# Performance work log

Hardware: AMD Instinct MI355X
Metric: run time of the kernel (lower is better)

The kernel has to match this reference:

```python
import jax, jax.numpy as jnp
import numpy as np
import math

HID, NH, NKV, HD = 2048, 16, 4, 128
GROUPS = NH // NKV

def fq(x, bits, axis=None):
    # symmetric fake-quant with straight-through rounding; per-tensor unless axis given
    qmax = 2.0 ** (bits - 1) - 1.0
    if axis is None:
        amax = jnp.max(jnp.abs(x))
    else:
        amax = jnp.max(jnp.abs(x), axis=axis, keepdims=True)
    scale = jnp.maximum(amax, 1e-8) / qmax
    q = jnp.clip(jnp.round(x / scale), -qmax - 1.0, qmax) * scale
    return x + jax.lax.stop_gradient(q - x)

def dyn_quant_linear(x, W, b, w_bits=8):
    # DynamicQuantLinear: per-out-channel weight fake-quant + dynamic per-tensor 8-bit act quant
    Wq = fq(W, w_bits, axis=1)          # W: [out, in]
    xq = fq(x, 8)
    y = xq @ Wq.T
    return y + b if b is not None else y

def fq_matmul(a, b, a_bits, b_bits):
    # FakeQuantMatmul
    return jnp.einsum('hqd,hdk->hqk', fq(a, a_bits), fq(b, b_bits))

def rotate_half(x):
    x1, x2 = jnp.split(x, 2, axis=-1)
    return jnp.concatenate([-x2, x1], axis=-1)

def setup_inputs() -> dict:
    key = jax.random.key(0)
    ks = jax.random.split(key, 12)
    inp = {
        'hidden_states': jax.random.normal(ks[0], (1, 512, HID), jnp.float32),
        'cos': jax.random.uniform(ks[1], (1, 512, HD), jnp.float32),
        'sin': jax.random.uniform(ks[2], (1, 512, HD), jnp.float32),
        'cache_k': jax.random.normal(ks[3], (NKV, 8192, HD), jnp.float32),
        'cache_v': jax.random.normal(ks[4], (NKV, 8192, HD), jnp.float32),
        'mask': jnp.zeros((1, 512, 8192), jnp.float32),
        'Wq': jax.random.normal(ks[5], (NH * HD, HID), jnp.float32) * 0.02,
        'bq': jnp.zeros((NH * HD,), jnp.float32),
        'Wk': jax.random.normal(ks[6], (NKV * HD, HID), jnp.float32) * 0.02,
        'bk': jnp.zeros((NKV * HD,), jnp.float32),
        'Wv': jax.random.normal(ks[7], (NKV * HD, HID), jnp.float32) * 0.02,
        'bv': jnp.zeros((NKV * HD,), jnp.float32),
        'Wo': jax.random.normal(ks[8], (HID, NH * HD), jnp.float32) * 0.02,
    }
    return inp

def reference(hidden_states, cos, sin, cache_k, cache_v, mask, Wq, bq, Wk, bk, Wv, bv, Wo):
    # ConstFakeQuant on incoming caches
    cache_k = fq(cache_k, 8)
    cache_v = fq(cache_v, 8)
    seqlen = hidden_states.shape[1]
    x = hidden_states.reshape(seqlen, HID)  # batch_size == 1
    q = dyn_quant_linear(x, Wq, bq).reshape(seqlen, NH, HD).transpose(1, 0, 2)    # [NH,S,D]
    k = dyn_quant_linear(x, Wk, bk).reshape(seqlen, NKV, HD).transpose(1, 0, 2)   # [NKV,S,D]
    v = dyn_quant_linear(x, Wv, bv).reshape(seqlen, NKV, HD).transpose(1, 0, 2)   # [NKV,S,D]
    # RoPE
    q = q * cos + rotate_half(q) * sin
    k = k * cos + rotate_half(k) * sin
    c_len = cache_k.shape[1]
    # sliding KV cache: drop oldest seqlen, append new
    cache_k = jnp.concatenate([cache_k[:, seqlen:, :], k], axis=1)   # [NKV,c_len,D]
    cache_v = jnp.concatenate([cache_v[:, seqlen:, :], v], axis=1)
    kT = cache_k.transpose(0, 2, 1)                                   # [NKV,D,c_len]
    q4 = q.reshape(NKV, GROUPS * seqlen, HD)
    attn = fq_matmul(q4, kT, 8, 8)                                    # [NKV,G*S,c_len]
    attn = attn.reshape(NH, seqlen, c_len) / math.sqrt(HD)
    attn = attn + mask
    attn = jax.nn.softmax(attn, axis=-1)
    attn = attn.reshape(NKV, GROUPS * seqlen, c_len)
    out = fq_matmul(attn, cache_v, 8, 8)                              # sv: [NKV,G*S,D]
    out = out.reshape(NH, seqlen, HD).transpose(1, 0, 2).reshape(1, seqlen, HID)
    out = dyn_quant_linear(out.reshape(seqlen, HID), Wo, None).reshape(1, seqlen, HID)
    # cache outputs re-fake-quantized
    k_out = fq(k, 8)
    v_out = fq(v, 8)
    return (out, k_out, v_out)
```

## Files before the change

kernel.cpp:

```cpp
#include <hip/hip_runtime.h>
#include <math.h>

#define S_LEN 512
#define HID 2048
#define NH 16
#define NKV 4
#define HD 128
#define CL 8192
#define TAILN (CL - S_LEN)
#define NKO (NKV * S_LEN * HD)
#define KS1 16
#define KCH1 (CL / KS1)
#define KS2 8
#define KCH2 (CL / KS2)
#define INV_SQRT_HD 0.08838834764831845f

typedef unsigned short u16;
typedef __attribute__((ext_vector_type(8))) unsigned short u16x8;
typedef __attribute__((ext_vector_type(4))) unsigned short u16x4;
typedef __attribute__((ext_vector_type(8))) short bf16x8;
typedef __attribute__((ext_vector_type(4))) float f32x4;

enum {
  SC_AMAX_X = 0, SC_AMAX_CK, SC_AMAX_CK_TAIL, SC_AMAX_CV, SC_AMAX_CV_TAIL,
  SC_AMAX_Q, SC_AMAX_K, SC_AMAX_V, SC_AMAX_AO, SC_MIN_L,
  SC_NUM
};

__device__ __forceinline__ float warpMax64(float v) {
  #pragma unroll
  for (int o = 32; o; o >>= 1) v = fmaxf(v, __shfl_down(v, o, 64));
  return v;
}
__device__ __forceinline__ float warpMin64(float v) {
  #pragma unroll
  for (int o = 32; o; o >>= 1) v = fminf(v, __shfl_down(v, o, 64));
  return v;
}
__device__ __forceinline__ float blockMax256(float v) {
  __shared__ float sm_[4];
  __syncthreads();
  v = warpMax64(v);
  if ((threadIdx.x & 63) == 0) sm_[threadIdx.x >> 6] = v;
  __syncthreads();
  return fmaxf(fmaxf(sm_[0], sm_[1]), fmaxf(sm_[2], sm_[3]));
}
__device__ __forceinline__ float blockMin256(float v) {
  __shared__ float sn_[4];
  __syncthreads();
  v = warpMin64(v);
  if ((threadIdx.x & 63) == 0) sn_[threadIdx.x >> 6] = v;
  __syncthreads();
  return fminf(fminf(sn_[0], sn_[1]), fminf(sn_[2], sn_[3]));
}
__device__ __forceinline__ void atomicMinPosF(float* a, float v) {
  atomicMin((unsigned int*)a, __float_as_uint(v));
}
__device__ __forceinline__ float clampq(float q) {
  return fminf(fmaxf(q, -128.f), 127.f);
}
__device__ __forceinline__ u16 bf16bits(float f) {
  return (u16)(__float_as_uint(f) >> 16);
}
__device__ __forceinline__ float mk_scale(float am) {
  return fmaxf(am, 1e-8f) / 127.f;
}
__device__ __forceinline__ void gl2lds16(const u16* g, u16* l) {
  __builtin_amdgcn_global_load_lds((const __attribute__((address_space(1))) void*)g,
                                   (__attribute__((address_space(3))) void*)l, 16, 0, 0);
}

__global__ __launch_bounds__(256) void k_pre(const float* __restrict__ hidden,
                                             const float* __restrict__ ck, const float* __restrict__ cv,
                                             float* __restrict__ pp) {
  int b = blockIdx.x, tid = threadIdx.x;
  if (b < 512) {
    const int n4 = S_LEN * HID / 4;
    float m = 0.f;
    const float4* x4 = (const float4*)hidden;
    for (int i = b * 256 + tid; i < n4; i += 512 * 256) {
      float4 v = x4[i];
      m = fmaxf(m, fmaxf(fmaxf(fabsf(v.x), fabsf(v.y)), fmaxf(fabsf(v.z), fabsf(v.w))));
    }
    m = blockMax256(m);
    if (tid == 0) pp[b] = m;
  } else {
    int isv = b >= 1024;
    int bb = b - (isv ? 1024 : 512);
    const float4* x4 = (const float4*)(isv ? cv : ck);
    const int n4 = NKV * CL * HD / 4;
    float mf = 0.f, mt = 0.f;
    for (int i = bb * 256 + tid; i < n4; i += 512 * 256) {
      float4 v = x4[i];
      float a = fmaxf(fmaxf(fabsf(v.x), fabsf(v.y)), fmaxf(fabsf(v.z), fabsf(v.w)));
      mf = fmaxf(mf, a);
      int t = (i >> 5) & (CL - 1);
      if (t >= S_LEN) mt = fmaxf(mt, a);
    }
    mf = blockMax256(mf);
    mt = blockMax256(mt);
    if (tid == 0) {
      pp[512 + isv * 1024 + bb] = mf;
      pp[1024 + isv * 1024 + bb] = mt;
    }
  }
}

__global__ __launch_bounds__(256) void k_reduce_pre(const float* __restrict__ pp, float* __restrict__ sc) {
  const int slots[5] = {SC_AMAX_X, SC_AMAX_CK, SC_AMAX_CK_TAIL, SC_AMAX_CV, SC_AMAX_CV_TAIL};
  if (threadIdx.x == 0) sc[SC_MIN_L] = INFINITY;
  #pragma unroll
  for (int r = 0; r < 5; r++) {
    float v = fmaxf(pp[r * 512 + threadIdx.x], pp[r * 512 + 256 + threadIdx.x]);
    v = blockMax256(v);
    if (threadIdx.x == 0) sc[slots[r]] = v;
  }
}

__global__ __launch_bounds__(256) void k_quant_w_all(const float* __restrict__ Wq, const float* __restrict__ Wk,
                                                     const float* __restrict__ Wv, const float* __restrict__ Wo,
                                                     u16* __restrict__ WQb, u16* __restrict__ WKb,
                                                     u16* __restrict__ WVb, u16* __restrict__ WOb,
                                                     float* __restrict__ SWq, float* __restrict__ SWk,
                                                     float* __restrict__ SWv, float* __restrict__ SWo) {
  int r = blockIdx.x;
  const float* W; u16* Wb; float* SW; int row;
  if (r < 2048)      { W = Wq; Wb = WQb; SW = SWq; row = r; }
  else if (r < 2560) { W = Wk; Wb = WKb; SW = SWk; row = r - 2048; }
  else if (r < 3072) { W = Wv; Wb = WVb; SW = SWv; row = r - 2560; }
  else               { W = Wo; Wb = WOb; SW = SWo; row = r - 3072; }
  size_t base = (size_t)row * HID;
  const float4* w4 = (const float4*)(W + base);
  const int n4 = HID / 4;
  float am = 0.f;
  for (int i = threadIdx.x; i < n4; i += 256) {
    float4 v = w4[i];
    am = fmaxf(am, fmaxf(fmaxf(fabsf(v.x), fabsf(v.y)), fmaxf(fabsf(v.z), fabsf(v.w))));
  }
  am = blockMax256(am);
  float s = fmaxf(am, 1e-8f) / 127.f;
  if (threadIdx.x == 0) SW[row] = s;
  for (int i = threadIdx.x; i < n4; i += 256) {
    float4 v = w4[i];
    u16x4 o;
    o[0] = bf16bits(clampq(rintf(v.x / s)));
    o[1] = bf16bits(clampq(rintf(v.y / s)));
    o[2] = bf16bits(clampq(rintf(v.z / s)));
    o[3] = bf16bits(clampq(rintf(v.w / s)));
    *(u16x4*)(Wb + base + (size_t)i * 4) = o;
  }
}

__global__ __launch_bounds__(256) void k_quant_act_b(const float* __restrict__ in, u16* __restrict__ outp,
                                                     int n4, const float* __restrict__ sc, int axslot) {
  float s = mk_scale(sc[axslot]);
  const float4* i4 = (const float4*)in;
  for (int i = blockIdx.x * 256 + threadIdx.x; i < n4; i += gridDim.x * 256) {
    float4 v = i4[i];
    u16x4 o;
    o[0] = bf16bits(clampq(rintf(v.x / s)));
    o[1] = bf16bits(clampq(rintf(v.y / s)));
    o[2] = bf16bits(clampq(rintf(v.z / s)));
    o[3] = bf16bits(clampq(rintf(v.w / s)));
    *(u16x4*)(outp + (size_t)i * 4) = o;
  }
}

__global__ __launch_bounds__(256) void k_quant_q(const float* __restrict__ QB, u16* __restrict__ QI,
                                                 const float* __restrict__ sc) {
  int idx = blockIdx.x * 256 + threadIdx.x;
  float s = mk_scale(sc[SC_AMAX_Q]);
  int e = idx * 4;
  int srow = e >> 11, rem = e & 2047;
  int h = rem >> 7, d = rem & 127;
  float4 v = *(const float4*)&QB[e];
  u16x4 o;
  o[0] = bf16bits(clampq(rintf(v.x / s)));
  o[1] = bf16bits(clampq(rintf(v.y / s)));
  o[2] = bf16bits(clampq(rintf(v.z / s)));
  o[3] = bf16bits(clampq(rintf(v.w / s)));
  *(u16x4*)(QI + ((size_t)h * S_LEN + srow) * HD + d) = o;
}

__global__ __launch_bounds__(256) void k_gemm_qkv(const u16* __restrict__ A,
                                                  const u16* __restrict__ WQb, const u16* __restrict__ WKb,
                                                  const u16* __restrict__ WVb,
                                                  const float* __restrict__ SWq, const float* __restrict__ SWk,
                                                  const float* __restrict__ SWv,
                                                  const float* __restrict__ bq, const float* __restrict__ bk,
                                                  const float* __restrict__ bv,
                                                  const float* __restrict__ sc,
                                                  float* __restrict__ QB, float* __restrict__ KB,
                                                  float* __restrict__ VB) {
  __shared__ u16 Al[64 * 64];
  __shared__ u16 Bl[64 * 64];
  int bx = blockIdx.x;
  const u16* B; const float* SW; const float* bias; float* C; int N, c0;
  if (bx < 32)      { B = WQb; SW = SWq; bias = bq; C = QB; N = HID; c0 = bx * 64; }
  else if (bx < 40) { B = WKb; SW = SWk; bias = bk; C = KB; N = NKV * HD; c0 = (bx - 32) * 64; }
  else              { B = WVb; SW = SWv; bias = bv; C = VB; N = NKV * HD; c0 = (bx - 40) * 64; }
  int tid = threadIdx.x, lane = tid & 63, w = tid >> 6;
  int g = lane >> 4, c = lane & 15;
  int wy = w >> 1, wx = w & 1;
  int r0 = blockIdx.y * 64;
  float sx = mk_scale(sc[SC_AMAX_X]);
  f32x4 acc[2][2] = {};
  for (int k0 = 0; k0 < HID; k0 += 64) {
    __syncthreads();
    #pragma unroll
    for (int i = 0; i < 2; i++) {
      int b = tid + i * 256;
      int row = b >> 3, c8d = b & 7, c8s = c8d ^ (row & 7);
      gl2lds16(A + (size_t)(r0 + row) * HID + k0 + c8s * 8, Al + b * 8);
    }
    #pragma unroll
    for (int i = 0; i < 2; i++) {
      int b = tid + i * 256;
      int row = b >> 3, c8d = b & 7, c8s = c8d ^ (row & 7);
      gl2lds16(B + (size_t)(c0 + row) * HID + k0 + c8s * 8, Bl + b * 8);
    }
    __syncthreads();
    #pragma unroll
    for (int ks = 0; ks < 2; ks++) {
      bf16x8 af[2], bf[2];
      #pragma unroll
      for (int a = 0; a < 2; a++) {
        int row = wy * 32 + a * 16 + c;
        af[a] = *(const bf16x8*)(Al + row * 64 + (((4 * ks + g) ^ (row & 7)) * 8));
      }
      #pragma unroll
      for (int b = 0; b < 2; b++) {
        int row = wx * 32 + b * 16 + c;
        bf[b] = *(const bf16x8*)(Bl + row * 64 + (((4 * ks + g) ^ (row & 7)) * 8));
      }
      #pragma unroll
      for (int a = 0; a < 2; a++)
        #pragma unroll
        for (int b = 0; b < 2; b++)
          acc[a][b] = __builtin_amdgcn_mfma_f32_16x16x32_bf16(af[a], bf[b], acc[a][b], 0, 0, 0);
    }
  }
  #pragma unroll
  for (int a = 0; a < 2; a++)
    #pragma unroll
    for (int b = 0; b < 2; b++) {
      int col = c0 + wx * 32 + b * 16 + c;
      float sca = sx * SW[col];
      float bs = bias[col];
      #pragma unroll
      for (int r = 0; r < 4; r++) {
        int row = r0 + wy * 32 + a * 16 + 4 * g + r;
        C[(size_t)row * N + col] = acc[a][b][r] * sca + bs;
      }
    }
}

__global__ __launch_bounds__(256) void k_gemm_q(const u16* __restrict__ A, const u16* __restrict__ B,
                                                const float* __restrict__ SW, const float* __restrict__ sc,
                                                int axslot, float* __restrict__ C, int M, int N, int K) {
  __shared__ u16 Al[64 * 64];
  __shared__ u16 Bl[64 * 64];
  int tid = threadIdx.x, lane = tid & 63, w = tid >> 6;
  int g = lane >> 4, c = lane & 15;
  int wy = w >> 1, wx = w & 1;
  int r0 = blockIdx.y * 64, c0 = blockIdx.x * 64;
  float sx = mk_scale(sc[axslot]);
  f32x4 acc[2][2] = {};
  for (int k0 = 0; k0 < K; k0 += 64) {
    __syncthreads();
    #pragma unroll
    for (int i = 0; i < 2; i++) {
      int b = tid + i * 256;
      int row = b >> 3, c8d = b & 7, c8s = c8d ^ (row & 7);
      gl2lds16(A + (size_t)(r0 + row) * K + k0 + c8s * 8, Al + b * 8);
    }
    #pragma unroll
    for (int i = 0; i < 2; i++) {
      int b = tid + i * 256;
      int row = b >> 3, c8d = b & 7, c8s = c8d ^ (row & 7);
      gl2lds16(B + (size_t)(c0 + row) * K + k0 + c8s * 8, Bl + b * 8);
    }
    __syncthreads();
    #pragma unroll
    for (int ks = 0; ks < 2; ks++) {
      bf16x8 af[2], bf[2];
      #pragma unroll
      for (int a = 0; a < 2; a++) {
        int row = wy * 32 + a * 16 + c;
        af[a] = *(const bf16x8*)(Al + row * 64 + (((4 * ks + g) ^ (row & 7)) * 8));
      }
      #pragma unroll
      for (int b = 0; b < 2; b++) {
        int row = wx * 32 + b * 16 + c;
        bf[b] = *(const bf16x8*)(Bl + row * 64 + (((4 * ks + g) ^ (row & 7)) * 8));
      }
      #pragma unroll
      for (int a = 0; a < 2; a++)
        #pragma unroll
        for (int b = 0; b < 2; b++)
          acc[a][b] = __builtin_amdgcn_mfma_f32_16x16x32_bf16(af[a], bf[b], acc[a][b], 0, 0, 0);
    }
  }
  #pragma unroll
  for (int a = 0; a < 2; a++)
    #pragma unroll
    for (int b = 0; b < 2; b++) {
      int col = c0 + wx * 32 + b * 16 + c;
      float sca = sx * SW[col];
      #pragma unroll
      for (int r = 0; r < 4; r++) {
        int row = r0 + wy * 32 + a * 16 + 4 * g + r;
        C[(size_t)row * N + col] = acc[a][b][r] * sca;
      }
    }
}

__global__ __launch_bounds__(256) void k_rope_amax(float* __restrict__ QB, float* __restrict__ KB,
                                                   const float* __restrict__ VB,
                                                   const float* __restrict__ cosb, const float* __restrict__ sinb,
                                                   float* __restrict__ PR) {
  const int nQ = S_LEN * NH * 64;
  const int nK = S_LEN * NKV * 64;
  int idx = blockIdx.x * 256 + threadIdx.x;
  float am = 0.f;
  if (idx < nQ) {
    int s = idx >> 10, rem = idx & 1023, h = rem >> 6, d = rem & 63;
    float c1 = cosb[s * HD + d], s1 = sinb[s * HD + d];
    float c2 = cosb[s * HD + d + 64], s2 = sinb[s * HD + d + 64];
    float* p = &QB[(size_t)s * (NH * HD) + h * HD + d];
    float x1 = p[0], x2 = p[64];
    float y1 = x1 * c1 - x2 * s1;
    float y2 = x2 * c2 + x1 * s2;
    p[0] = y1; p[64] = y2;
    am = fmaxf(fabsf(y1), fabsf(y2));
  } else if (idx < nQ + nK) {
    int j = idx - nQ;
    int s = j >> 8, rem = j & 255, h = rem >> 6, d = rem & 63;
    float c1 = cosb[s * HD + d], s1 = sinb[s * HD + d];
    float c2 = cosb[s * HD + d + 64], s2 = sinb[s * HD + d + 64];
    float* p = &KB[(size_t)s * (NKV * HD) + h * HD + d];
    float x1 = p[0], x2 = p[64];
    float y1 = x1 * c1 - x2 * s1;
    float y2 = x2 * c2 + x1 * s2;
    p[0] = y1; p[64] = y2;
    am = fmaxf(fabsf(y1), fabsf(y2));
  } else {
    int j = idx - nQ - nK;
    float4 v = ((const float4*)VB)[j];
    am = fmaxf(fmaxf(fabsf(v.x), fabsf(v.y)), fmaxf(fabsf(v.z), fabsf(v.w)));
  }
  am = blockMax256(am);
  if (threadIdx.x == 0) PR[blockIdx.x] = am;
}

__global__ __launch_bounds__(256) void k_reduce_rope(const float* __restrict__ PR, float* __restrict__ sc) {
  float v = 0.f;
  #pragma unroll
  for (int i = 0; i < 8; i++) v = fmaxf(v, PR[threadIdx.x + 256 * i]);
  v = blockMax256(v);
  if (threadIdx.x == 0) sc[SC_AMAX_Q] = v;
  v = fmaxf(PR[2048 + threadIdx.x], PR[2048 + 256 + threadIdx.x]);
  v = blockMax256(v);
  if (threadIdx.x == 0) sc[SC_AMAX_K] = v;
  v = PR[2560 + threadIdx.x];
  v = blockMax256(v);
  if (threadIdx.x == 0) sc[SC_AMAX_V] = v;
}

__global__ __launch_bounds__(256) void k_build_cache2(const float* __restrict__ ck, const float* __restrict__ cv,
                                                      const float* __restrict__ KB, const float* __restrict__ VB,
                                                      u16* __restrict__ KCb, u16* __restrict__ VCb,
                                                      u16* __restrict__ VT, float* __restrict__ dout,
                                                      const float* __restrict__ sc) {
  __shared__ u16 T[64][140];
  int b = blockIdx.x;
  int isv = b >= NKV * 128;
  int bb = b - isv * NKV * 128;
  int kvh = bb >> 7, tb = bb & 127;
  float s1 = mk_scale(sc[isv ? SC_AMAX_CV : SC_AMAX_CK]);
  float tq = fminf(rintf(sc[isv ? SC_AMAX_CV_TAIL : SC_AMAX_CK_TAIL] / s1), 127.f) * s1;
  float s2 = fmaxf(fmaxf(tq, sc[isv ? SC_AMAX_V : SC_AMAX_K]), 1e-8f) / 127.f;
  float so = mk_scale(sc[isv ? SC_AMAX_V : SC_AMAX_K]);
  const float* cache = isv ? cv : ck;
  const float* fresh = isv ? VB : KB;
  u16* Cb = isv ? VCb : KCb;
  int tid = threadIdx.x;
  int t0 = tb * 64;
  #pragma unroll
  for (int i = 0; i < 8; i++) {
    int idx = tid + i * 256;
    int t = idx >> 5, d4 = (idx & 31) << 2;
    int tt = t0 + t;
    float4 x;
    float q0_, q1_, q2_, q3_;
    if (tt < TAILN) {
      x = *(const float4*)&cache[((size_t)kvh * CL + tt + S_LEN) * HD + d4];
      q0_ = clampq(rintf(clampq(rintf(x.x / s1)) * s1 / s2));
      q1_ = clampq(rintf(clampq(rintf(x.y / s1)) * s1 / s2));
      q2_ = clampq(rintf(clampq(rintf(x.z / s1)) * s1 / s2));
      q3_ = clampq(rintf(clampq(rintf(x.w / s1)) * s1 / s2));
    } else {
      x = *(const float4*)&fresh[(size_t)(tt - TAILN) * (NKV * HD) + kvh * HD + d4];
      q0_ = clampq(rintf(x.x / s2));
      q1_ = clampq(rintf(x.y / s2));
      q2_ = clampq(rintf(x.z / s2));
      q3_ = clampq(rintf(x.w / s2));
      float4 o;
      o.x = clampq(rintf(x.x / so)) * so;
      o.y = clampq(rintf(x.y / so)) * so;
      o.z = clampq(rintf(x.z / so)) * so;
      o.w = clampq(rintf(x.w / so)) * so;
      *(float4*)&dout[(size_t)S_LEN * HID + (size_t)isv * NKO +
                      ((size_t)kvh * S_LEN + (tt - TAILN)) * HD + d4] = o;
    }
    u16x4 ov;
    ov[0] = bf16bits(q0_); ov[1] = bf16bits(q1_); ov[2] = bf16bits(q2_); ov[3] = bf16bits(q3_);
    *(u16x4*)(Cb + ((size_t)kvh * CL + tt) * HD + d4) = ov;
    if (isv) *(u16x4*)&T[t][d4] = ov;
  }
  if (isv) {
    __syncthreads();
    #pragma unroll
    for (int i = 0; i < 4; i++) {
      int j = tid + i * 256;
      int d = j >> 3, tc = (j & 7) << 3;
      u16x8 v;
      #pragma unroll
      for (int k = 0; k < 8; k++) v[k] = T[tc + k][d];
      *(u16x8*)(VT + ((size_t)kvh * HD + d) * CL + t0 + tc) = v;
    }
  }
}

__global__ __launch_bounds__(256) void k_mattn1(const u16* __restrict__ QI, const u16* __restrict__ KCb,
                                                const float* __restrict__ mask, const float* __restrict__ sc,
                                                float* __restrict__ PM, float* __restrict__ PL) {
  __shared__ u16 Kl[2][64 * HD];
  int bid = blockIdx.x;
  int wki = (bid & 7) * (NH * 8 * KS1 / 8) + (bid >> 3);
  int kc = wki >> 7, rem2 = wki & 127, qb = rem2 >> 4, h = rem2 & 15, kv = h >> 2;
  int tid = threadIdx.x, lane = tid & 63, wv = tid >> 6, g = lane >> 4, c = lane & 15;
  float sq  = mk_scale(sc[SC_AMAX_Q]);
  float sck = mk_scale(sc[SC_AMAX_CK]);
  float tqk = fminf(rintf(sc[SC_AMAX_CK_TAIL] / sck), 127.f) * sck;
  float skn = fmaxf(fmaxf(tqk, sc[SC_AMAX_K]), 1e-8f) / 127.f;
  float sscale = sq * skn * INV_SQRT_HD;
  int q0 = qb * 64 + wv * 16;
  bf16x8 qf[4];
  {
    const u16* qrow = QI + ((size_t)h * S_LEN + q0 + c) * HD + g * 8;
    #pragma unroll
    for (int ds = 0; ds < 4; ds++) qf[ds] = *(const bf16x8*)(qrow + 32 * ds);
  }
  float m[4], l[4];
  #pragma unroll
  for (int r = 0; r < 4; r++) { m[r] = -INFINITY; l[r] = 0.f; }
  int qlane = q0 + 4 * g;
  int kbase0 = kc * KCH1;
  const u16* Kg = KCb + (size_t)kv * CL * HD;
  auto stage = [&](int buf, int kbase) {
    #pragma unroll
    for (int i = 0; i < 4; i++) {
      int b = tid + i * 256;
      int row = b >> 4, c8d = b & 15, c8s = c8d ^ (row & 7);
      gl2lds16(Kg + (size_t)(kbase + row) * HD + c8s * 8, Kl[buf] + b * 8);
    }
  };
  stage(0, kbase0);
  __syncthreads();
  int cur = 0;
  for (int kb = 0; kb < KCH1; kb += 64) {
    int kbase = kbase0 + kb;
    if (kb + 64 < KCH1) stage(cur ^ 1, kbase + 64);
    f32x4 sc4[4];
    #pragma unroll
    for (int kf = 0; kf < 4; kf++) {
      f32x4 s4 = {0.f, 0.f, 0.f, 0.f};
      int krow = kf * 16 + c;
      #pragma unroll
      for (int ds = 0; ds < 4; ds++) {
        bf16x8 kf8 = *(const bf16x8*)(Kl[cur] + krow * HD + (((4 * ds + g) ^ (krow & 7)) * 8));
        s4 = __builtin_amdgcn_mfma_f32_16x16x32_bf16(qf[ds], kf8, s4, 0, 0, 0);
      }
      sc4[kf] = s4;
    }
    #pragma unroll
    for (int r = 0; r < 4; r++) {
      const float* mr = mask + (size_t)(qlane + r) * CL + kbase;
      float v0 = fmaf(sc4[0][r], sscale, mr[c]);
      float v1 = fmaf(sc4[1][r], sscale, mr[16 + c]);
      float v2 = fmaf(sc4[2][r], sscale, mr[32 + c]);
      float v3 = fmaf(sc4[3][r], sscale, mr[48 + c]);
      float tmax = fmaxf(fmaxf(v0, v1), fmaxf(v2, v3));
      float nm = fmaxf(m[r], tmax);
      float e0 = __expf(v0 - nm), e1 = __expf(v1 - nm);
      float e2 = __expf(v2 - nm), e3 = __expf(v3 - nm);
      float f = __expf(m[r] - nm);
      l[r] = fmaf(l[r], f, (e0 + e1) + (e2 + e3));
      m[r] = nm;
    }
    __syncthreads();
    cur ^= 1;
  }
  #pragma unroll
  for (int r = 0; r < 4; r++) {
    #pragma unroll
    for (int off = 1; off < 16; off <<= 1) {
      float om = __shfl_xor(m[r], off, 64);
      float ol = __shfl_xor(l[r], off, 64);
      float nm = fmaxf(m[r], om);
      l[r] = l[r] * __expf(m[r] - nm) + ol * __expf(om - nm);
      m[r] = nm;
    }
  }
  if (c == 0) {
    size_t base = ((size_t)kc * NH + h) * S_LEN + qlane;
    #pragma unroll
    for (int r = 0; r < 4; r++) { PM[base + r] = m[r]; PL[base + r] = l[r]; }
  }
}

__global__ __launch_bounds__(256) void k_merge4(const float* __restrict__ PM, const float* __restrict__ PL,
                                                float* __restrict__ MLm, float* __restrict__ MLl, float* sc) {
  int idx = blockIdx.x * 256 + threadIdx.x;
  const int st = NH * S_LEN;
  float m = PM[idx];
  #pragma unroll
  for (int p = 1; p < KS1; p++) m = fmaxf(m, PM[p * st + idx]);
  float l = 0.f;
  #pragma unroll
  for (int p = 0; p < KS1; p++) l += PL[p * st + idx] * __expf(PM[p * st + idx] - m);
  MLm[idx] = m; MLl[idx] = l;
  float lm = blockMin256(l);
  if (threadIdx.x == 0) atomicMinPosF(&sc[SC_MIN_L], lm);
}

__global__ __launch_bounds__(256) void k_mattn2(const u16* __restrict__ QI, const u16* __restrict__ KCb,
                                                const u16* __restrict__ VT, const float* __restrict__ mask,
                                                const float* __restrict__ sc, const float* __restrict__ MLm,
                                                const float* __restrict__ MLl, float* __restrict__ AOp) {
  __shared__ u16 Kl[2][64 * HD];
  __shared__ u16 Vl[2][HD * 64];
  __shared__ u16 Pl[4 * 16 * 64];
  int bid = blockIdx.x;
  int wki = (bid & 7) * (NH * 8 * KS2 / 8) + (bid >> 3);
  int kc = wki >> 7, rem2 = wki & 127, qb = rem2 >> 4, h = rem2 & 15, kv = h >> 2;
  int tid = threadIdx.x, lane = tid & 63, wv = tid >> 6, g = lane >> 4, c = lane & 15;
  float sq  = mk_scale(sc[SC_AMAX_Q]);
  float sck = mk_scale(sc[SC_AMAX_CK]);
  float tqk = fminf(rintf(sc[SC_AMAX_CK_TAIL] / sck), 127.f) * sck;
  float skn = fmaxf(fmaxf(tqk, sc[SC_AMAX_K]), 1e-8f) / 127.f;
  float sscale = sq * skn * INV_SQRT_HD;
  float scv = mk_scale(sc[SC_AMAX_CV]);
  float tqv = fminf(rintf(sc[SC_AMAX_CV_TAIL] / scv), 127.f) * scv;
  float svn = fmaxf(fmaxf(tqv, sc[SC_AMAX_V]), 1e-8f) / 127.f;
  float sp  = mk_scale(1.0f / sc[SC_MIN_L]);
  float rsp = 1.0f / sp;
  float psv = sp * svn;
  int q0 = qb * 64 + wv * 16;
  bf16x8 qf[4];
  {
    const u16* qrow = QI + ((size_t)h * S_LEN + q0 + c) * HD + g * 8;
    #pragma unroll
    for (int ds = 0; ds < 4; ds++) qf[ds] = *(const bf16x8*)(qrow + 32 * ds);
  }
  int qlane = q0 + 4 * g;
  float mreg[4], cvl[4];
  #pragma unroll
  for (int r = 0; r < 4; r++) {
    mreg[r] = MLm[h * S_LEN + qlane + r];
    cvl[r] = rsp / MLl[h * S_LEN + qlane + r];
  }
  f32x4 acc[8] = {};
  const u16* Kg = KCb + (size_t)kv * CL * HD;
  const u16* Vg = VT + (size_t)kv * HD * CL;
  int kbase0 = kc * KCH2;
  u16* Pw = Pl + wv * 1024;
  auto stage = [&](int buf, int kbase) {
    #pragma unroll
    for (int i = 0; i < 4; i++) {
      int b = tid + i * 256;
      int row = b >> 4, c8d = b & 15, c8s = c8d ^ (row & 7);
      gl2lds16(Kg + (size_t)(kbase + row) * HD + c8s * 8, Kl[buf] + b * 8);
    }
    #pragma unroll
    for (int i = 0; i < 4; i++) {
      int b = tid + i * 256;
      int row = b >> 3, c8d = b & 7, c8s = c8d ^ (row & 7);
      gl2lds16(Vg + (size_t)row * CL + kbase + c8s * 8, Vl[buf] + b * 8);
    }
  };
  stage(0, kbase0);
  __syncthreads();
  int cur = 0;
  for (int kb = 0; kb < KCH2; kb += 64) {
    int kbase = kbase0 + kb;
    if (kb + 64 < KCH2) stage(cur ^ 1, kbase + 64);
    #pragma unroll
    for (int kf = 0; kf < 4; kf++) {
      f32x4 s4 = {0.f, 0.f, 0.f, 0.f};
      int krow = kf * 16 + c;
      #pragma unroll
      for (int ds = 0; ds < 4; ds++) {
        bf16x8 kf8 = *(const bf16x8*)(Kl[cur] + krow * HD + (((4 * ds + g) ^ (krow & 7)) * 8));
        s4 = __builtin_amdgcn_mfma_f32_16x16x32_bf16(qf[ds], kf8, s4, 0, 0, 0);
      }
      int key = kbase + kf * 16 + c;
      #pragma unroll
      for (int r = 0; r < 4; r++) {
        float v = fmaf(s4[r], sscale, mask[(size_t)(qlane + r) * CL + key]);
        float pi = fminf(rintf(__expf(v - mreg[r]) * cvl[r]), 127.f);
        int prow = 4 * g + r, pcol = kf * 16 + c;
        Pw[prow * 64 + (pcol ^ ((prow & 7) << 3))] = bf16bits(pi);
      }
    }
    asm volatile("s_waitcnt lgkmcnt(0)" ::: "memory");
    __builtin_amdgcn_sched_barrier(0);
    bf16x8 pa[2];
    #pragma unroll
    for (int s = 0; s < 2; s++)
      pa[s] = *(const bf16x8*)(Pw + c * 64 + ((32 * s + 8 * g) ^ ((c & 7) << 3)));
    #pragma unroll
    for (int dt = 0; dt < 8; dt++) {
      #pragma unroll
      for (int s = 0; s < 2; s++) {
        int drow = dt * 16 + c;
        bf16x8 vf = *(const bf16x8*)(Vl[cur] + drow * 64 + (((4 * s + g) ^ (drow & 7)) * 8));
        acc[dt] = __builtin_amdgcn_mfma_f32_16x16x32_bf16(pa[s], vf, acc[dt], 0, 0, 0);
      }
    }
    __syncthreads();
    cur ^= 1;
  }
  float* outp = AOp + (size_t)kc * S_LEN * HID;
  #pragma unroll
  for (int dt = 0; dt < 8; dt++)
    #pragma unroll
    for (int r = 0; r < 4; r++)
      outp[(size_t)(qlane + r) * HID + h * HD + dt * 16 + c] = acc[dt][r] * psv;
}

__global__ __launch_bounds__(256) void k_combine_ao(const float* __restrict__ AOp, float* __restrict__ AO,
                                                    float* __restrict__ PA) {
  int idx = blockIdx.x * 256 + threadIdx.x;
  const int st = S_LEN * HID / 4;
  const f32x4* p4 = (const f32x4*)AOp;
  f32x4 a = p4[idx];
  #pragma unroll
  for (int p = 1; p < KS2; p++) {
    f32x4 b = p4[p * st + idx];
    a = a + b;
  }
  *((f32x4*)AO + idx) = a;
  float am = fmaxf(fmaxf(fabsf(a[0]), fabsf(a[1])), fmaxf(fabsf(a[2]), fabsf(a[3])));
  am = blockMax256(am);
  if (threadIdx.x == 0) PA[blockIdx.x] = am;
}

__global__ __launch_bounds__(256) void k_reduce_ao(const float* __restrict__ PA, float* __restrict__ sc) {
  float v = 0.f;
  #pragma unroll
  for (int i = 0; i < 4; i++) v = fmaxf(v, PA[threadIdx.x + 256 * i]);
  v = blockMax256(v);
  if (threadIdx.x == 0) sc[SC_AMAX_AO] = v;
}

extern "C" void kernel_launch(void* const* d_in, const int* in_sizes, int n_in,
                              void* d_out, int out_size, void* d_ws, size_t ws_size,
                              hipStream_t stream) {
  const float* hidden = (const float*)d_in[0];
  const float* cosb   = (const float*)d_in[1];
  const float* sinb   = (const float*)d_in[2];
  const float* cachek = (const float*)d_in[3];
  const float* cachev = (const float*)d_in[4];
  const float* mask   = (const float*)d_in[5];
  const float* Wq     = (const float*)d_in[6];
  const float* bq     = (const float*)d_in[7];
  const float* Wk     = (const float*)d_in[8];
  const float* bk     = (const float*)d_in[9];
  const float* Wv     = (const float*)d_in[10];
  const float* bv     = (const float*)d_in[11];
  const float* Wo     = (const float*)d_in[12];
  float* out = (float*)d_out;

  char* base = (char*)d_ws;
  auto alloc = [&](size_t bytes) { char* p = base; base += (bytes + 255) & ~(size_t)255; return p; };

  float* SC  = (float*)alloc(64 * 4);
  float* PP  = (float*)alloc(2560 * 4);
  float* PR  = (float*)alloc(2816 * 4);
  float* PA  = (float*)alloc(1024 * 4);
  float* SWq = (float*)alloc(HID * 4);
  float* SWk = (float*)alloc(NKV * HD * 4);
  float* SWv = (float*)alloc(NKV * HD * 4);
  float* SWo = (float*)alloc(HID * 4);
  u16* XI    = (u16*)alloc((size_t)S_LEN * HID * 2);
  u16* WQb   = (u16*)alloc((size_t)HID * HID * 2);
  u16* WKb   = (u16*)alloc((size_t)NKV * HD * HID * 2);
  u16* WVb   = (u16*)alloc((size_t)NKV * HD * HID * 2);
  u16* WOb   = (u16*)alloc((size_t)HID * HID * 2);
  float* QB  = (float*)alloc((size_t)S_LEN * HID * 4);
  float* KB  = (float*)alloc((size_t)S_LEN * NKV * HD * 4);
  float* VB  = (float*)alloc((size_t)S_LEN * NKV * HD * 4);
  u16* KCb   = (u16*)alloc((size_t)NKV * CL * HD * 2);
  u16* VCb   = (u16*)alloc((size_t)NKV * CL * HD * 2);
  u16* VT    = (u16*)alloc((size_t)NKV * HD * CL * 2);
  u16* QI    = (u16*)alloc((size_t)NH * S_LEN * HD * 2);
  float* PM  = (float*)alloc((size_t)KS1 * NH * S_LEN * 4);
  float* PL  = (float*)alloc((size_t)KS1 * NH * S_LEN * 4);
  float* MLm = (float*)alloc((size_t)NH * S_LEN * 4);
  float* MLl = (float*)alloc((size_t)NH * S_LEN * 4);
  float* AOp = (float*)alloc((size_t)KS2 * S_LEN * HID * 4);
  float* AO  = (float*)alloc((size_t)S_LEN * HID * 4);
  u16* AOi   = (u16*)alloc((size_t)S_LEN * HID * 2);

  k_pre<<<1536, 256, 0, stream>>>(hidden, cachek, cachev, PP);
  k_reduce_pre<<<1, 256, 0, stream>>>(PP, SC);
  k_quant_w_all<<<5120, 256, 0, stream>>>(Wq, Wk, Wv, Wo, WQb, WKb, WVb, WOb, SWq, SWk, SWv, SWo);
  k_quant_act_b<<<1024, 256, 0, stream>>>(hidden, XI, S_LEN * HID / 4, SC, SC_AMAX_X);
  {
    dim3 g(48, S_LEN / 64);
    k_gemm_qkv<<<g, 256, 0, stream>>>(XI, WQb, WKb, WVb, SWq, SWk, SWv, bq, bk, bv, SC, QB, KB, VB);
  }
  k_rope_amax<<<2816, 256, 0, stream>>>(QB, KB, VB, cosb, sinb, PR);
  k_reduce_rope<<<1, 256, 0, stream>>>(PR, SC);
  k_build_cache2<<<NKV * 128 * 2, 256, 0, stream>>>(cachek, cachev, KB, VB, KCb, VCb, VT, out, SC);
  k_quant_q<<<1024, 256, 0, stream>>>(QB, QI, SC);
  k_mattn1<<<NH * 8 * KS1, 256, 0, stream>>>(QI, KCb, mask, SC, PM, PL);
  k_merge4<<<NH * S_LEN / 256, 256, 0, stream>>>(PM, PL, MLm, MLl, SC);
  k_mattn2<<<NH * 8 * KS2, 256, 0, stream>>>(QI, KCb, VT, mask, SC, MLm, MLl, AOp);
  k_combine_ao<<<1024, 256, 0, stream>>>(AOp, AO, PA);
  k_reduce_ao<<<1, 256, 0, stream>>>(PA, SC);
  k_quant_act_b<<<1024, 256, 0, stream>>>(AO, AOi, S_LEN * HID / 4, SC, SC_AMAX_AO);
  {
    dim3 g(HID / 64, S_LEN / 64);
    k_gemm_q<<<g, 256, 0, stream>>>(AOi, WOb, SWo, SC, SC_AMAX_AO, out, S_LEN, HID, HID);
  }
  (void)in_sizes; (void)n_in; (void)out_size; (void)ws_size;
}
```

Measured before the change: 210.9 us.

## Double-buffer projection GEMMs, unroll attention loops by two, halve PV key splits

Projection GEMMs now double-buffer their LDS tiles so the next K tile loads while the current one is in MFMA. Both attention kernels get a manually unrolled ping-pong loop with static buffer indices and hoisted mask row pointers. The PV kernel's key split count drops from 8 to 4, which halves the partial output buffers and combine traffic but launches fewer blocks. Weight quantization is specialised to exactly two float4 per thread. k_gemm_q now loops over HID instead of K, which is only correct while K equals HID.

Measured after the change: 211.6 us. Within noise of the previous version (+0.4%).

```diff
diff --git a/kernel.cpp b/kernel.cpp
--- a/kernel.cpp
+++ b/kernel.cpp
@@ -11,7 +11,7 @@
 #define NKO (NKV * S_LEN * HD)
 #define KS1 16
 #define KCH1 (CL / KS1)
-#define KS2 8
+#define KS2 4
 #define KCH2 (CL / KS2)
 #define INV_SQRT_HD 0.08838834764831845f
 
@@ -131,24 +131,25 @@
   else               { W = Wo; Wb = WOb; SW = SWo; row = r - 3072; }
   size_t base = (size_t)row * HID;
   const float4* w4 = (const float4*)(W + base);
-  const int n4 = HID / 4;
-  float am = 0.f;
-  for (int i = threadIdx.x; i < n4; i += 256) {
-    float4 v = w4[i];
-    am = fmaxf(am, fmaxf(fmaxf(fabsf(v.x), fabsf(v.y)), fmaxf(fabsf(v.z), fabsf(v.w))));
-  }
+  int tid = threadIdx.x;
+  float4 va = w4[tid];
+  float4 vb = w4[tid + 256];
+  float am = fmaxf(fmaxf(fmaxf(fabsf(va.x), fabsf(va.y)), fmaxf(fabsf(va.z), fabsf(va.w))),
+                   fmaxf(fmaxf(fabsf(vb.x), fabsf(vb.y)), fmaxf(fabsf(vb.z), fabsf(vb.w))));
   am = blockMax256(am);
   float s = fmaxf(am, 1e-8f) / 127.f;
-  if (threadIdx.x == 0) SW[row] = s;
-  for (int i = threadIdx.x; i < n4; i += 256) {
-    float4 v = w4[i];
-    u16x4 o;
-    o[0] = bf16bits(clampq(rintf(v.x / s)));
-    o[1] = bf16bits(clampq(rintf(v.y / s)));
-    o[2] = bf16bits(clampq(rintf(v.z / s)));
-    o[3] = bf16bits(clampq(rintf(v.w / s)));
-    *(u16x4*)(Wb + base + (size_t)i * 4) = o;
-  }
+  if (tid == 0) SW[row] = s;
+  u16x4 oa, ob;
+  oa[0] = bf16bits(clampq(rintf(va.x / s)));
+  oa[1] = bf16bits(clampq(rintf(va.y / s)));
+  oa[2] = bf16bits(clampq(rintf(va.z / s)));
+  oa[3] = bf16bits(clampq(rintf(va.w / s)));
+  ob[0] = bf16bits(clampq(rintf(vb.x / s)));
+  ob[1] = bf16bits(clampq(rintf(vb.y / s)));
+  ob[2] = bf16bits(clampq(rintf(vb.z / s)));
+  ob[3] = bf16bits(clampq(rintf(vb.w / s)));
+  *(u16x4*)(Wb + base + (size_t)tid * 4) = oa;
+  *(u16x4*)(Wb + base + (size_t)(tid + 256) * 4) = ob;
 }
 
 __global__ __launch_bounds__(256) void k_quant_act_b(const float* __restrict__ in, u16* __restrict__ outp,
@@ -182,6 +183,45 @@
   *(u16x4*)(QI + ((size_t)h * S_LEN + srow) * HD + d) = o;
 }
 
+#define GQ_STAGE(BUF, K0)                                                          \
+  {                                                                                \
+    _Pragma("unroll")                                                              \
+    for (int i = 0; i < 2; i++) {                                                  \
+      int b = tid + i * 256;                                                       \
+      int row = b >> 3, c8d = b & 7, c8s = c8d ^ (row & 7);                        \
+      gl2lds16(A + (size_t)(r0 + row) * HID + (K0) + c8s * 8, Al[BUF] + b * 8);    \
+    }                                                                              \
+    _Pragma("unroll")                                                              \
+    for (int i = 0; i < 2; i++) {                                                  \
+      int b = tid + i * 256;                                                       \
+      int row = b >> 3, c8d = b & 7, c8s = c8d ^ (row & 7);                        \
+      gl2lds16(B + (size_t)(c0 + row) * HID + (K0) + c8s * 8, Bl[BUF] + b * 8);    \
+    }                                                                              \
+  }
+
+#define GQ_TILE(BUF)                                                               \
+  {                                                                                \
+    _Pragma("unroll")                                                              \
+    for (int ks = 0; ks < 2; ks++) {                                               \
+      bf16x8 af[2], bfr[2];                                                        \
+      _Pragma("unroll")                                                            \
+      for (int a = 0; a < 2; a++) {                                                \
+        int row = wy * 32 + a * 16 + c;                                            \
+        af[a] = *(const bf16x8*)(Al[BUF] + row * 64 + (((4 * ks + g) ^ (row & 7)) * 8)); \
+      }                                                                            \
+      _Pragma("unroll")                                                            \
+      for (int b2 = 0; b2 < 2; b2++) {                                             \
+        int row = wx * 32 + b2 * 16 + c;                                           \
+        bfr[b2] = *(const bf16x8*)(Bl[BUF] + row * 64 + (((4 * ks + g) ^ (row & 7)) * 8)); \
+      }                                                                            \
+      _Pragma("unroll")                                                            \
+      for (int a = 0; a < 2; a++)                                                  \
+        _Pragma("unroll")                                                          \
+        for (int b2 = 0; b2 < 2; b2++)                                             \
+          acc[a][b2] = __builtin_amdgcn_mfma_f32_16x16x32_bf16(af[a], bfr[b2], acc[a][b2], 0, 0, 0); \
+    }                                                                              \
+  }
+
 __global__ __launch_bounds__(256) void k_gemm_qkv(const u16* __restrict__ A,
                                                   const u16* __restrict__ WQb, const u16* __restrict__ WKb,
                                                   const u16* __restrict__ WVb,
@@ -192,8 +232,8 @@
                                                   const float* __restrict__ sc,
                                                   float* __restrict__ QB, float* __restrict__ KB,
                                                   float* __restrict__ VB) {
-  __shared__ u16 Al[64 * 64];
-  __shared__ u16 Bl[64 * 64];
+  __shared__ u16 Al[2][64 * 64];
+  __shared__ u16 Bl[2][64 * 64];
   int bx = blockIdx.x;
   const u16* B; const float* SW; const float* bias; float* C; int N, c0;
   if (bx < 32)      { B = WQb; SW = SWq; bias = bq; C = QB; N = HID; c0 = bx * 64; }
@@ -205,52 +245,27 @@
   int r0 = blockIdx.y * 64;
   float sx = mk_scale(sc[SC_AMAX_X]);
   f32x4 acc[2][2] = {};
-  for (int k0 = 0; k0 < HID; k0 += 64) {
-    __syncthreads();
-    #pragma unroll
-    for (int i = 0; i < 2; i++) {
-      int b = tid + i * 256;
-      int row = b >> 3, c8d = b & 7, c8s = c8d ^ (row & 7);
-      gl2lds16(A + (size_t)(r0 + row) * HID + k0 + c8s * 8, Al + b * 8);
-    }
-    #pragma unroll
-    for (int i = 0; i < 2; i++) {
-      int b = tid + i * 256;
-      int row = b >> 3, c8d = b & 7, c8s = c8d ^ (row & 7);
-      gl2lds16(B + (size_t)(c0 + row) * HID + k0 + c8s * 8, Bl + b * 8);
-    }
-    __syncthreads();
-    #pragma unroll
-    for (int ks = 0; ks < 2; ks++) {
-      bf16x8 af[2], bf[2];
-      #pragma unroll
-      for (int a = 0; a < 2; a++) {
-        int row = wy * 32 + a * 16 + c;
-        af[a] = *(const bf16x8*)(Al + row * 64 + (((4 * ks + g) ^ (row & 7)) * 8));
-      }
-      #pragma unroll
-      for (int b = 0; b < 2; b++) {
-        int row = wx * 32 + b * 16 + c;
-        bf[b] = *(const bf16x8*)(Bl + row * 64 + (((4 * ks + g) ^ (row & 7)) * 8));
-      }
-      #pragma unroll
-      for (int a = 0; a < 2; a++)
-        #pragma unroll
-        for (int b = 0; b < 2; b++)
-          acc[a][b] = __builtin_amdgcn_mfma_f32_16x16x32_bf16(af[a], bf[b], acc[a][b], 0, 0, 0);
-    }
+  GQ_STAGE(0, 0)
+  __syncthreads();
+  for (int k0 = 0; k0 < HID; k0 += 128) {
+    GQ_STAGE(1, k0 + 64)
+    GQ_TILE(0)
+    __syncthreads();
+    if (k0 + 128 < HID) GQ_STAGE(0, k0 + 128)
+    GQ_TILE(1)
+    __syncthreads();
   }
   #pragma unroll
   for (int a = 0; a < 2; a++)
     #pragma unroll
-    for (int b = 0; b < 2; b++) {
-      int col = c0 + wx * 32 + b * 16 + c;
+    for (int b2 = 0; b2 < 2; b2++) {
+      int col = c0 + wx * 32 + b2 * 16 + c;
       float sca = sx * SW[col];
       float bs = bias[col];
       #pragma unroll
       for (int r = 0; r < 4; r++) {
         int row = r0 + wy * 32 + a * 16 + 4 * g + r;
-        C[(size_t)row * N + col] = acc[a][b][r] * sca + bs;
+        C[(size_t)row * N + col] = acc[a][b2][r] * sca + bs;
       }
     }
 }
@@ -258,59 +273,34 @@
 __global__ __launch_bounds__(256) void k_gemm_q(const u16* __restrict__ A, const u16* __restrict__ B,
                                                 const float* __restrict__ SW, const float* __restrict__ sc,
                                                 int axslot, float* __restrict__ C, int M, int N, int K) {
-  __shared__ u16 Al[64 * 64];
-  __shared__ u16 Bl[64 * 64];
+  __shared__ u16 Al[2][64 * 64];
+  __shared__ u16 Bl[2][64 * 64];
   int tid = threadIdx.x, lane = tid & 63, w = tid >> 6;
   int g = lane >> 4, c = lane & 15;
   int wy = w >> 1, wx = w & 1;
   int r0 = blockIdx.y * 64, c0 = blockIdx.x * 64;
   float sx = mk_scale(sc[axslot]);
   f32x4 acc[2][2] = {};
-  for (int k0 = 0; k0 < K; k0 += 64) {
-    __syncthreads();
-    #pragma unroll
-    for (int i = 0; i < 2; i++) {
-      int b = tid + i * 256;
-      int row = b >> 3, c8d = b & 7, c8s = c8d ^ (row & 7);
-      gl2lds16(A + (size_t)(r0 + row) * K + k0 + c8s * 8, Al + b * 8);
-    }
-    #pragma unroll
-    for (int i = 0; i < 2; i++) {
-      int b = tid + i * 256;
-      int row = b >> 3, c8d = b & 7, c8s = c8d ^ (row & 7);
-      gl2lds16(B + (size_t)(c0 + row) * K + k0 + c8s * 8, Bl + b * 8);
-    }
-    __syncthreads();
-    #pragma unroll
-    for (int ks = 0; ks < 2; ks++) {
-      bf16x8 af[2], bf[2];
-      #pragma unroll
-      for (int a = 0; a < 2; a++) {
-        int row = wy * 32 + a * 16 + c;
-        af[a] = *(const bf16x8*)(Al + row * 64 + (((4 * ks + g) ^ (row & 7)) * 8));
-      }
-      #pragma unroll
-      for (int b = 0; b < 2; b++) {
-        int row = wx * 32 + b * 16 + c;
-        bf[b] = *(const bf16x8*)(Bl + row * 64 + (((4 * ks + g) ^ (row & 7)) * 8));
-      }
-      #pragma unroll
-      for (int a = 0; a < 2; a++)
-        #pragma unroll
-        for (int b = 0; b < 2; b++)
-          acc[a][b] = __builtin_amdgcn_mfma_f32_16x16x32_bf16(af[a], bf[b], acc[a][b], 0, 0, 0);
-    }
+  GQ_STAGE(0, 0)
+  __syncthreads();
+  for (int k0 = 0; k0 < HID; k0 += 128) {
+    GQ_STAGE(1, k0 + 64)
+    GQ_TILE(0)
+    __syncthreads();
+    if (k0 + 128 < HID) GQ_STAGE(0, k0 + 128)
+    GQ_TILE(1)
+    __syncthreads();
   }
   #pragma unroll
   for (int a = 0; a < 2; a++)
     #pragma unroll
-    for (int b = 0; b < 2; b++) {
-      int col = c0 + wx * 32 + b * 16 + c;
+    for (int b2 = 0; b2 < 2; b2++) {
+      int col = c0 + wx * 32 + b2 * 16 + c;
       float sca = sx * SW[col];
       #pragma unroll
       for (int r = 0; r < 4; r++) {
         int row = r0 + wy * 32 + a * 16 + 4 * g + r;
-        C[(size_t)row * N + col] = acc[a][b][r] * sca;
+        C[(size_t)row * N + col] = acc[a][b2][r] * sca;
       }
     }
 }
@@ -432,6 +422,48 @@
   }
 }
 
+#define M1_STAGE(BUF, KBASE)                                                       \
+  {                                                                                \
+    const u16* kgt = Kg + (size_t)(KBASE) * HD;                                    \
+    _Pragma("unroll")                                                              \
+    for (int i = 0; i < 4; i++) {                                                  \
+      int b = tid + i * 256;                                                       \
+      int row = b >> 4, c8d = b & 15, c8s = c8d ^ (row & 7);                       \
+      gl2lds16(kgt + row * HD + c8s * 8, Kl[BUF] + b * 8);                         \
+    }                                                                              \
+  }
+
+#define M1_TILE(BUF, KBASE)                                                        \
+  {                                                                                \
+    const int kbase_ = (KBASE);                                                    \
+    f32x4 sc4[4];                                                                  \
+    _Pragma("unroll")                                                              \
+    for (int kf = 0; kf < 4; kf++) {                                               \
+      f32x4 s4 = {0.f, 0.f, 0.f, 0.f};                                             \
+      int krow = kf * 16 + c;                                                      \
+      _Pragma("unroll")                                                            \
+      for (int ds = 0; ds < 4; ds++) {                                             \
+        bf16x8 kf8 = *(const bf16x8*)(Kl[BUF] + krow * HD + (((4 * ds + g) ^ (krow & 7)) * 8)); \
+        s4 = __builtin_amdgcn_mfma_f32_16x16x32_bf16(qf[ds], kf8, s4, 0, 0, 0);    \
+      }                                                                            \
+      sc4[kf] = s4;                                                                \
+    }                                                                              \
+    _Pragma("unroll")                                                              \
+    for (int r = 0; r < 4; r++) {                                                  \
+      float v0 = fmaf(sc4[0][r], sscale, mrb[r * CL + kbase_ + c]);                \
+      float v1 = fmaf(sc4[1][r], sscale, mrb[r * CL + kbase_ + 16 + c]);           \
+      float v2 = fmaf(sc4[2][r], sscale, mrb[r * CL + kbase_ + 32 + c]);           \
+      float v3 = fmaf(sc4[3][r], sscale, mrb[r * CL + kbase_ + 48 + c]);           \
+      float tmax = fmaxf(fmaxf(v0, v1), fmaxf(v2, v3));                            \
+      float nm = fmaxf(m[r], tmax);                                                \
+      float e0 = __expf(v0 - nm), e1 = __expf(v1 - nm);                            \
+      float e2 = __expf(v2 - nm), e3 = __expf(v3 - nm);                            \
+      float f = __expf(m[r] - nm);                                                 \
+      l[r] = fmaf(l[r], f, (e0 + e1) + (e2 + e3));                                 \
+      m[r] = nm;                                                                   \
+    }                                                                              \
+  }
+
 __global__ __launch_bounds__(256) void k_mattn1(const u16* __restrict__ QI, const u16* __restrict__ KCb,
                                                 const float* __restrict__ mask, const float* __restrict__ sc,
                                                 float* __restrict__ PM, float* __restrict__ PL) {
@@ -458,49 +490,16 @@
   int qlane = q0 + 4 * g;
   int kbase0 = kc * KCH1;
   const u16* Kg = KCb + (size_t)kv * CL * HD;
-  auto stage = [&](int buf, int kbase) {
-    #pragma unroll
-    for (int i = 0; i < 4; i++) {
-      int b = tid + i * 256;
-      int row = b >> 4, c8d = b & 15, c8s = c8d ^ (row & 7);
-      gl2lds16(Kg + (size_t)(kbase + row) * HD + c8s * 8, Kl[buf] + b * 8);
-    }
-  };
-  stage(0, kbase0);
+  const float* mrb = mask + (size_t)qlane * CL;
+  M1_STAGE(0, kbase0)
   __syncthreads();
-  int cur = 0;
-  for (int kb = 0; kb < KCH1; kb += 64) {
-    int kbase = kbase0 + kb;
-    if (kb + 64 < KCH1) stage(cur ^ 1, kbase + 64);
-    f32x4 sc4[4];
-    #pragma unroll
-    for (int kf = 0; kf < 4; kf++) {
-      f32x4 s4 = {0.f, 0.f, 0.f, 0.f};
-      int krow = kf * 16 + c;
-      #pragma unroll
-      for (int ds = 0; ds < 4; ds++) {
-        bf16x8 kf8 = *(const bf16x8*)(Kl[cur] + krow * HD + (((4 * ds + g) ^ (krow & 7)) * 8));
-        s4 = __builtin_amdgcn_mfma_f32_16x16x32_bf16(qf[ds], kf8, s4, 0, 0, 0);
-      }
-      sc4[kf] = s4;
-    }
-    #pragma unroll
-    for (int r = 0; r < 4; r++) {
-      const float* mr = mask + (size_t)(qlane + r) * CL + kbase;
-      float v0 = fmaf(sc4[0][r], sscale, mr[c]);
-      float v1 = fmaf(sc4[1][r], sscale, mr[16 + c]);
-      float v2 = fmaf(sc4[2][r], sscale, mr[32 + c]);
-      float v3 = fmaf(sc4[3][r], sscale, mr[48 + c]);
-      float tmax = fmaxf(fmaxf(v0, v1), fmaxf(v2, v3));
-      float nm = fmaxf(m[r], tmax);
-      float e0 = __expf(v0 - nm), e1 = __expf(v1 - nm);
-      float e2 = __expf(v2 - nm), e3 = __expf(v3 - nm);
-      float f = __expf(m[r] - nm);
-      l[r] = fmaf(l[r], f, (e0 + e1) + (e2 + e3));
-      m[r] = nm;
-    }
-    __syncthreads();
-    cur ^= 1;
+  for (int kb = 0; kb < KCH1; kb += 128) {
+    M1_STAGE(1, kbase0 + kb + 64)
+    M1_TILE(0, kbase0 + kb)
+    __syncthreads();
+    if (kb + 128 < KCH1) M1_STAGE(0, kbase0 + kb + 128)
+    M1_TILE(1, kbase0 + kb + 64)
+    __syncthreads();
   }
   #pragma unroll
   for (int r = 0; r < 4; r++) {
@@ -534,6 +533,58 @@
   float lm = blockMin256(l);
   if (threadIdx.x == 0) atomicMinPosF(&sc[SC_MIN_L], lm);
 }
+
+#define M2_STAGE(BUF, KBASE)                                                       \
+  {                                                                                \
+    const u16* kgt = Kg + (size_t)(KBASE) * HD;                                    \
+    const u16* vgt = Vg + (KBASE);                                                 \
+    _Pragma("unroll")                                                              \
+    for (int i = 0; i < 4; i++) {                                                  \
+      int b = tid + i * 256;                                                       \
+      int row = b >> 4, c8d = b & 15, c8s = c8d ^ (row & 7);                       \
+      gl2lds16(kgt + row * HD + c8s * 8, Kl[BUF] + b * 8);                         \
+    }                                                                              \
+    _Pragma("unroll")                                                              \
+    for (int i = 0; i < 4; i++) {                                                  \
+      int b = tid + i * 256;                                                       \
+      int row = b >> 3, c8d = b & 7, c8s = c8d ^ (row & 7);                        \
+      gl2lds16(vgt + (size_t)row * CL + c8s * 8, Vl[BUF] + b * 8);                 \
+    }                                                                              \
+  }
+
+#define M2_TILE(BUF, KBASE)                                                        \
+  {                                                                                \
+    const int kbase_ = (KBASE);                                                    \
+    _Pragma("unroll")                                                              \
+    for (int kf = 0; kf < 4; kf++) {                                               \
+      f32x4 s4 = {0.f, 0.f, 0.f, 0.f};                                             \
+      int krow = kf * 16 + c;                                                      \
+      _Pragma("unroll")                                                            \
+      for (int ds = 0; ds < 4; ds++) {                                             \
+        bf16x8 kf8 = *(const bf16x8*)(Kl[BUF] + krow * HD + (((4 * ds + g) ^ (krow & 7)) * 8)); \
+        s4 = __builtin_amdgcn_mfma_f32_16x16x32_bf16(qf[ds], kf8, s4, 0, 0, 0);    \
+      }                                                                            \
+      _Pragma("unroll")                                                            \
+      for (int r = 0; r < 4; r++) {                                                \
+        float v = fmaf(s4[r], sscale, mrb[r * CL + kbase_ + kf * 16 + c]);         \
+        float pi = fminf(rintf(__expf(v - mreg[r]) * cvl[r]), 127.f);              \
+        int prow = 4 * g + r, pcol = kf * 16 + c;                                  \
+        Pw[prow * 64 + (pcol ^ ((prow & 7) << 3))] = bf16bits(pi);                 \
+      }                                                                            \
+    }                                                                              \
+    asm volatile("s_waitcnt lgkmcnt(0)" ::: "memory");                             \
+    __builtin_amdgcn_sched_barrier(0);                                             \
+    bf16x8 pa0 = *(const bf16x8*)(Pw + c * 64 + ((8 * g) ^ ((c & 7) << 3)));       \
+    bf16x8 pa1 = *(const bf16x8*)(Pw + c * 64 + ((32 + 8 * g) ^ ((c & 7) << 3)));  \
+    _Pragma("unroll")                                                              \
+    for (int dt = 0; dt < 8; dt++) {                                               \
+      int drow = dt * 16 + c;                                                      \
+      bf16x8 vf0 = *(const bf16x8*)(Vl[BUF] + drow * 64 + ((g ^ (drow & 7)) * 8)); \
+      acc[dt] = __builtin_amdgcn_mfma_f32_16x16x32_bf16(pa0, vf0, acc[dt], 0, 0, 0); \
+      bf16x8 vf1 = *(const bf16x8*)(Vl[BUF] + drow * 64 + (((4 + g) ^ (drow & 7)) * 8)); \
+      acc[dt] = __builtin_amdgcn_mfma_f32_16x16x32_bf16(pa1, vf1, acc[dt], 0, 0, 0); \
+    }                                                                              \
+  }
 
 __global__ __launch_bounds__(256) void k_mattn2(const u16* __restrict__ QI, const u16* __restrict__ KCb,
                                                 const u16* __restrict__ VT, const float* __restrict__ mask,
@@ -574,63 +625,18 @@
   f32x4 acc[8] = {};
   const u16* Kg = KCb + (size_t)kv * CL * HD;
   const u16* Vg = VT + (size_t)kv * HD * CL;
+  const float* mrb = mask + (size_t)qlane * CL;
   int kbase0 = kc * KCH2;
   u16* Pw = Pl + wv * 1024;
-  auto stage = [&](int buf, int kbase) {
-    #pragma unroll
-    for (int i = 0; i < 4; i++) {
-      int b = tid + i * 256;
-      int row = b >> 4, c8d = b & 15, c8s = c8d ^ (row & 7);
-      gl2lds16(Kg + (size_t)(kbase + row) * HD + c8s * 8, Kl[buf] + b * 8);
-    }
-    #pragma unroll
-    for (int i = 0; i < 4; i++) {
-      int b = tid + i * 256;
-      int row = b >> 3, c8d = b & 7, c8s = c8d ^ (row & 7);
-      gl2lds16(Vg + (size_t)row * CL + kbase + c8s * 8, Vl[buf] + b * 8);
-    }
-  };
-  stage(0, kbase0);
+  M2_STAGE(0, kbase0)
   __syncthreads();
-  int cur = 0;
-  for (int kb = 0; kb < KCH2; kb += 64) {
-    int kbase = kbase0 + kb;
-    if (kb + 64 < KCH2) stage(cur ^ 1, kbase + 64);
-    #pragma unroll
-    for (int kf = 0; kf < 4; kf++) {
-      f32x4 s4 = {0.f, 0.f, 0.f, 0.f};
-      int krow = kf * 16 + c;
-      #pragma unroll
-      for (int ds = 0; ds < 4; ds++) {
-        bf16x8 kf8 = *(const bf16x8*)(Kl[cur] + krow * HD + (((4 * ds + g) ^ (krow & 7)) * 8));
-        s4 = __builtin_amdgcn_mfma_f32_16x16x32_bf16(qf[ds], kf8, s4, 0, 0, 0);
-      }
-      int key = kbase + kf * 16 + c;
-      #pragma unroll
-      for (int r = 0; r < 4; r++) {
-        float v = fmaf(s4[r], sscale, mask[(size_t)(qlane + r) * CL + key]);
-        float pi = fminf(rintf(__expf(v - mreg[r]) * cvl[r]), 127.f);
-        int prow = 4 * g + r, pcol = kf * 16 + c;
-        Pw[prow * 64 + (pcol ^ ((prow & 7) << 3))] = bf16bits(pi);
-      }
-    }
-    asm volatile("s_waitcnt lgkmcnt(0)" ::: "memory");
-    __builtin_amdgcn_sched_barrier(0);
-    bf16x8 pa[2];
-    #pragma unroll
-    for (int s = 0; s < 2; s++)
-      pa[s] = *(const bf16x8*)(Pw + c * 64 + ((32 * s + 8 * g) ^ ((c & 7) << 3)));
-    #pragma unroll
-    for (int dt = 0; dt < 8; dt++) {
-      #pragma unroll
-      for (int s = 0; s < 2; s++) {
-        int drow = dt * 16 + c;
-        bf16x8 vf = *(const bf16x8*)(Vl[cur] + drow * 64 + (((4 * s + g) ^ (drow & 7)) * 8));
-        acc[dt] = __builtin_amdgcn_mfma_f32_16x16x32_bf16(pa[s], vf, acc[dt], 0, 0, 0);
-      }
-    }
-    __syncthreads();
-    cur ^= 1;
+  for (int kb = 0; kb < KCH2; kb += 128) {
+    M2_STAGE(1, kbase0 + kb + 64)
+    M2_TILE(0, kbase0 + kb)
+    __syncthreads();
+    if (kb + 128 < KCH2) M2_STAGE(0, kbase0 + kb + 128)
+    M2_TILE(1, kbase0 + kb + 64)
+    __syncthreads();
   }
   float* outp = AOp + (size_t)kc * S_LEN * HID;
   #pragma unroll
```
